# Optimization experiments

Measured on AMD Instinct MI355X. Metric: run time of the kernel, lower is better.

## Reference

```python
import jax, jax.numpy as jnp
import numpy as np

NEG = -1e9  # additive mask value


def _longformer_attn(x, kv_mask, Wq, bq, Wk, bk, Wv, bv, Wqg, bqg, Wkg, bkg, Wvg, bvg, Wo, bo, H, w, G):
    # x: [B, S, E]; kv_mask: [B, S] (mask*-1 > 0 => global; first G tokens are global by construction)
    B, S, E = x.shape
    D = E // H
    scale = 1.0 / float(D) ** 0.5

    def proj(W, b):  # -> [B, H, S, D]
        return (x @ W + b).reshape(B, S, H, D).transpose(0, 2, 1, 3)

    q = proj(Wq, bq) * scale
    k = proj(Wk, bk)
    v = proj(Wv, bv)

    nc = S // w  # number of query chunks of size w
    # banded keys/values: each chunk of w queries sees a 3w key band (prev/cur/next chunk)
    idx = (jnp.arange(nc) * w)[:, None] + jnp.arange(3 * w)[None, :]  # [nc, 3w] into padded seq

    def band(t):  # [B,H,S,D] -> [B,H,nc,3w,D]
        tp = jnp.pad(t, ((0, 0), (0, 0), (w, w), (0, 0)))
        return tp[:, :, idx, :]

    k3, v3 = band(k), band(v)
    qc = q.reshape(B, H, nc, w, D)
    s_win = jnp.einsum('bhcwd,bhced->bhcwe', qc, k3)  # [B,H,nc,w,3w]

    i = jnp.arange(w)[:, None]
    j = jnp.arange(3 * w)[None, :]
    rel_ok = (j >= i) & (j <= i + 2 * w)  # |key_pos - query_pos| <= w
    keypos = (jnp.arange(nc) * w)[:, None, None] + (jnp.arange(3 * w) - w)[None, None, :]  # [nc,1,3w]
    ok = rel_ok[None] & (keypos >= 0) & (keypos < S) & (keypos >= G)  # global keys handled separately
    s_win = jnp.where(ok[None, None], s_win, NEG)

    # every query also attends to the G global keys (standard projections)
    s_g = jnp.einsum('bhqd,bhgd->bhqg', q, k[:, :, :G])  # [B,H,S,G]
    s_all = jnp.concatenate([s_g, s_win.reshape(B, H, S, 3 * w)], axis=-1)
    p = jax.nn.softmax(s_all, axis=-1)  # joint softmax over global + window keys
    p_g, p_w = p[..., :G], p[..., G:].reshape(B, H, nc, w, 3 * w)

    out = jnp.einsum('bhcwe,bhced->bhcwd', p_w, v3).reshape(B, H, S, D)
    out = out + jnp.einsum('bhqg,bhgd->bhqd', p_g, v[:, :, :G])

    # global query rows: full attention over all tokens with the *global* projections
    qg = (x @ Wqg + bqg).reshape(B, S, H, D).transpose(0, 2, 1, 3)[:, :, :G] * scale
    kg = (x @ Wkg + bkg).reshape(B, S, H, D).transpose(0, 2, 1, 3)
    vg = (x @ Wvg + bvg).reshape(B, S, H, D).transpose(0, 2, 1, 3)
    pg = jax.nn.softmax(jnp.einsum('bhgd,bhsd->bhgs', qg, kg), axis=-1)  # [B,H,G,S]
    out = out.at[:, :, :G].set(jnp.einsum('bhgs,bhsd->bhgd', pg, vg))

    ctx = out.transpose(0, 2, 1, 3).reshape(B, S, E)
    return ctx @ Wo + bo  # wrapper's self.output Linear


def setup_inputs() -> dict:
    key = jax.random.key(0)
    B, S, E, H, w, G = 2, 4096, 1024, 16, 256, 64
    ks = jax.random.split(key, 20)
    x = jax.random.normal(ks[0], (B, S, E), dtype=jnp.float32)
    # key_value_states acts as the mask source: (kv * -1) > 0 marks global tokens
    kv = jnp.zeros((B, S), dtype=jnp.float32).at[:, :G].set(-1.0)

    def lin(k1, k2):
        return (jax.random.normal(k1, (E, E), dtype=jnp.float32) * 0.02,
                jax.random.normal(k2, (E,), dtype=jnp.float32) * 0.02)

    Wq, bq = lin(ks[1], ks[2])
    Wk, bk = lin(ks[3], ks[4])
    Wv, bv = lin(ks[5], ks[6])
    Wqg, bqg = lin(ks[7], ks[8])
    Wkg, bkg = lin(ks[9], ks[10])
    Wvg, bvg = lin(ks[11], ks[12])
    Wo, bo = lin(ks[13], ks[14])
    return {"hidden_states": x, "key_value_states": kv,
            "Wq": Wq, "bq": bq, "Wk": Wk, "bk": bk, "Wv": Wv, "bv": bv,
            "Wqg": Wqg, "bqg": bqg, "Wkg": Wkg, "bkg": bkg, "Wvg": Wvg, "bvg": bvg,
            "Wo": Wo, "bo": bo, "num_heads": H, "window": w, "num_global": G}


def reference(hidden_states, key_value_states, Wq, bq, Wk, bk, Wv, bv, Wqg, bqg, Wkg, bkg, Wvg, bvg, Wo, bo, num_heads, window, num_global):
    return _longformer_attn(hidden_states, key_value_states, Wq, bq, Wk, bk, Wv, bv,
                            Wqg, bqg, Wkg, bkg, Wvg, bvg, Wo, bo,
                            num_heads, window, num_global)
```

## Files before the change

### kernel.cpp

```cpp
#include <hip/hip_runtime.h>

typedef _Float16 half_t;
typedef _Float16 h8 __attribute__((ext_vector_type(8)));
typedef _Float16 h4 __attribute__((ext_vector_type(4)));
typedef _Float16 h2 __attribute__((ext_vector_type(2)));
typedef float f4 __attribute__((ext_vector_type(4)));

#define DEV __device__ __forceinline__

constexpr int Bc = 2, Sc = 4096, Ec = 1024, Hc = 16, Dc = 64, Wc = 256, Gc = 64;
constexpr float QSCALE = 0.125f;
constexpr float NEGV = -1e9f;

DEV f4 mfma16(h8 a, h8 b, f4 c) {
  return __builtin_amdgcn_mfma_f32_16x16x32_f16(a, b, c, 0, 0, 0);
}

DEV void gl_lds16(const half_t* g, half_t* l) {
  __builtin_amdgcn_global_load_lds((const __attribute__((address_space(1))) void*)g,
                                   (__attribute__((address_space(3))) void*)l, 16, 0, 0);
}

#define BARx() asm volatile("s_barrier" ::: "memory")
#define VMW(N) asm volatile("s_waitcnt vmcnt(" #N ")" ::: "memory")

__global__ void prep(const float* __restrict__ x,
                     const float* __restrict__ Wq, const float* __restrict__ Wk,
                     const float* __restrict__ Wv, const float* __restrict__ Wkg,
                     const float* __restrict__ Wvg, const float* __restrict__ Wqg,
                     const float* __restrict__ Wo,
                     half_t* __restrict__ xh, half_t* __restrict__ Wcat,
                     half_t* __restrict__ WtO) {
  __shared__ float tile[64][65];
  const int bx = blockIdx.x;
  if (bx < 4096) {
    const int i = bx * 256 + threadIdx.x;
    const float4* x4 = (const float4*)x;
    float4 a = x4[i * 2], b = x4[i * 2 + 1];
    h8 o;
    o[0] = (half_t)a.x; o[1] = (half_t)a.y; o[2] = (half_t)a.z; o[3] = (half_t)a.w;
    o[4] = (half_t)b.x; o[5] = (half_t)b.y; o[6] = (half_t)b.z; o[7] = (half_t)b.w;
    ((h8*)xh)[i] = o;
    return;
  }
  const int widx = bx - 4096;
  const int y = widx >> 8;
  const int xb = widx & 255;
  const float* W = (y == 0) ? Wq : (y == 1) ? Wk : (y == 2) ? Wv :
                   (y == 3) ? Wkg : (y == 4) ? Wvg : (y == 5) ? Wqg : Wo;
  half_t* Wt = (y < 6) ? (Wcat + (size_t)y * Ec * Ec) : WtO;
  const int bxt = xb & 15, byt = xb >> 4;
  const int tx = threadIdx.x & 63, ty = threadIdx.x >> 6;
  const int n0 = bxt * 64, k0 = byt * 64;
#pragma unroll
  for (int i = 0; i < 16; ++i) {
    int k = ty + i * 4;
    tile[k][tx] = W[(size_t)(k0 + k) * Ec + n0 + tx];
  }
  __syncthreads();
  const int tx2 = threadIdx.x & 31, ty2 = threadIdx.x >> 5;
#pragma unroll
  for (int i = 0; i < 8; ++i) {
    const int n = ty2 + i * 8;
    h2 v;
    v[0] = (half_t)tile[2 * tx2][n];
    v[1] = (half_t)tile[2 * tx2 + 1][n];
    *(h2*)(Wt + (size_t)(n0 + n) * Ec + k0 + tx2 * 2) = v;
  }
}

__global__ __launch_bounds__(256, 2) void gemm_proj(const half_t* __restrict__ A,
                                                    const half_t* __restrict__ Bt,
                                                    const float* __restrict__ bq,
                                                    const float* __restrict__ bk,
                                                    const float* __restrict__ bv,
                                                    const float* __restrict__ bkg,
                                                    const float* __restrict__ bvg,
                                                    const float* __restrict__ bqg,
                                                    half_t* __restrict__ qh, half_t* __restrict__ kh,
                                                    half_t* __restrict__ vt, half_t* __restrict__ kgh,
                                                    half_t* __restrict__ vgt, half_t* __restrict__ qgh) {
  __shared__ __align__(16) half_t Ash[3][8192];
  __shared__ __align__(16) half_t Bsh[3][4096];
  const bool qgblk = (blockIdx.y == 32);
  if (qgblk && blockIdx.x >= 8) return;
  const int tid = threadIdx.x;
  const int wv = tid >> 6, lane = tid & 63;
  const int mr = lane & 15, qd = lane >> 4;
  const int wv_m = wv >> 1, wv_n = wv & 1;
  const int col0 = qgblk ? (5 * Ec + (int)blockIdx.x * 128) : (int)blockIdx.x * 128;
  const int row0 = qgblk ? 0 : (int)blockIdx.y * 256;
  const int g = col0 >> 10;

  const half_t* sA[4];
  const half_t* sB[2];
  int dstoA[4], dstoB[2];
#pragma unroll
  for (int j = 0; j < 4; ++j) {
    const int slot = j * 256 + tid;
    const int r = slot >> 2;
    const int kc = (slot & 3) ^ ((r >> 1) & 3);
    int ar;
    if (qgblk) { const int rm = r & 127; ar = (rm < 64) ? rm : 4032 + rm; }
    else ar = row0 + r;
    sA[j] = A + (size_t)ar * Ec + kc * 8;
    dstoA[j] = slot * 8;
  }
#pragma unroll
  for (int j = 0; j < 2; ++j) {
    const int slot = j * 256 + tid;
    const int r = slot >> 2;
    const int kc = (slot & 3) ^ ((r >> 1) & 3);
    sB[j] = Bt + (size_t)(col0 + r) * Ec + kc * 8;
    dstoB[j] = slot * 8;
  }
  int aoff[8], boff[4];
#pragma unroll
  for (int mt = 0; mt < 8; ++mt) {
    const int r = wv_m * 128 + mt * 16 + mr;
    aoff[mt] = ((r << 2) | (qd ^ ((r >> 1) & 3))) * 8;
  }
#pragma unroll
  for (int nt = 0; nt < 4; ++nt) {
    const int r = wv_n * 64 + nt * 16 + mr;
    boff[nt] = ((r << 2) | (qd ^ ((r >> 1) & 3))) * 8;
  }

  f4 acc[8][4] = {};

  auto stage = [&](half_t* da, half_t* db, int k0) {
#pragma unroll
    for (int j = 0; j < 4; ++j) gl_lds16(sA[j] + k0, da + dstoA[j]);
#pragma unroll
    for (int j = 0; j < 2; ++j) gl_lds16(sB[j] + k0, db + dstoB[j]);
  };
  auto compute = [&](const half_t* ba, const half_t* bb) {
    h8 af[8], bf[4];
#pragma unroll
    for (int mt = 0; mt < 8; ++mt) af[mt] = *(const h8*)(ba + aoff[mt]);
#pragma unroll
    for (int nt = 0; nt < 4; ++nt) bf[nt] = *(const h8*)(bb + boff[nt]);
    __builtin_amdgcn_s_setprio(1);
#pragma unroll
    for (int mt = 0; mt < 8; ++mt)
#pragma unroll
      for (int nt = 0; nt < 4; ++nt)
        acc[mt][nt] = mfma16(af[mt], bf[nt], acc[mt][nt]);
    __builtin_amdgcn_s_setprio(0);
  };

  stage(&Ash[0][0], &Bsh[0][0], 0);
  stage(&Ash[1][0], &Bsh[1][0], 32);
  VMW(6);
  BARx();

#pragma unroll 1
  for (int it = 0; it < 10; ++it) {
    const int kk = it * 96;
    stage(&Ash[2][0], &Bsh[2][0], kk + 64);
    compute(&Ash[0][0], &Bsh[0][0]);
    VMW(6); BARx();
    stage(&Ash[0][0], &Bsh[0][0], kk + 96);
    compute(&Ash[1][0], &Bsh[1][0]);
    VMW(6); BARx();
    stage(&Ash[1][0], &Bsh[1][0], kk + 128);
    compute(&Ash[2][0], &Bsh[2][0]);
    VMW(6); BARx();
  }
  compute(&Ash[0][0], &Bsh[0][0]);
  VMW(0);
  BARx();
  compute(&Ash[1][0], &Bsh[1][0]);

  const float* bptr = (g == 0) ? bq : (g == 1) ? bk : (g == 2) ? bv :
                      (g == 3) ? bkg : (g == 4) ? bvg : bqg;
#pragma unroll
  for (int mt = 0; mt < 8; ++mt) {
#pragma unroll
    for (int nt = 0; nt < 4; ++nt) {
      const int C = col0 + wv_n * 64 + nt * 16 + mr;
      const int c1 = C & 1023, hh = c1 >> 6, d = c1 & 63;
      const float bval = bptr[c1];
      const int Rbase = row0 + wv_m * 128 + mt * 16 + qd * 4;
      f4 a = acc[mt][nt];
      if (g == 2 || g == 4) {
        half_t* O = (g == 2) ? vt : vgt;
        int b = Rbase >> 12, s = Rbase & 4095;
        h4 pk;
#pragma unroll
        for (int r = 0; r < 4; ++r) pk[r] = (half_t)(a[r] + bval);
        *(h4*)(O + ((size_t)(b * Hc + hh) * Dc + d) * Sc + s) = pk;
      } else if (g == 5) {
#pragma unroll
        for (int r = 0; r < 4; ++r) {
          int rr = Rbase + r;
          if (rr < 128) {
            int b = rr >> 6, s = rr & 63;
            qgh[((size_t)(b * Hc + hh) * Gc + s) * Dc + d] = (half_t)((a[r] + bval) * QSCALE);
          }
        }
      } else {
        half_t* O = (g == 0) ? qh : (g == 1) ? kh : kgh;
        const float scale = (g == 0) ? QSCALE : 1.0f;
#pragma unroll
        for (int r = 0; r < 4; ++r) {
          int R = Rbase + r;
          int b = R >> 12, s = R & 4095;
          O[((size_t)(b * Hc + hh) * Sc + s) * Dc + d] = (half_t)((a[r] + bval) * scale);
        }
      }
    }
  }
}

__global__ __launch_bounds__(256, 3) void gemm_out(const half_t* __restrict__ A,
                                                   const half_t* __restrict__ Bt,
                                                   const float* __restrict__ bias,
                                                   float* __restrict__ O) {
  __shared__ __align__(16) half_t Ash[3][4096];
  __shared__ __align__(16) half_t Bsh[3][4096];
  const int tid = threadIdx.x;
  const int wv = tid >> 6, lane = tid & 63;
  const int mr = lane & 15, qd = lane >> 4;
  const int wv_m = wv >> 1, wv_n = wv & 1;
  const int col0 = blockIdx.x * 128;
  const int row0 = blockIdx.y * 128;

  const half_t* sA[2];
  const half_t* sB[2];
  int dsto[2];
#pragma unroll
  for (int i = 0; i < 2; ++i) {
    const int slot = wv * 128 + i * 64 + lane;
    const int r = slot >> 2;
    const int kc = (slot & 3) ^ ((r >> 1) & 3);
    sA[i] = A + (size_t)(row0 + r) * Ec + kc * 8;
    sB[i] = Bt + (size_t)(col0 + r) * Ec + kc * 8;
    dsto[i] = (wv * 128 + i * 64) * 8;
  }
  int aoff[4], boff[4];
#pragma unroll
  for (int mt = 0; mt < 4; ++mt) {
    const int r = wv_m * 64 + mt * 16 + mr;
    aoff[mt] = ((r << 2) | (qd ^ ((r >> 1) & 3))) * 8;
  }
#pragma unroll
  for (int nt = 0; nt < 4; ++nt) {
    const int r = wv_n * 64 + nt * 16 + mr;
    boff[nt] = ((r << 2) | (qd ^ ((r >> 1) & 3))) * 8;
  }

  f4 acc[4][4] = {};

  auto stage = [&](half_t* da, half_t* db, int k0) {
#pragma unroll
    for (int i = 0; i < 2; ++i) {
      gl_lds16(sA[i] + k0, da + dsto[i]);
      gl_lds16(sB[i] + k0, db + dsto[i]);
    }
  };
  auto compute = [&](const half_t* ba, const half_t* bb) {
    h8 af[4], bf[4];
#pragma unroll
    for (int mt = 0; mt < 4; ++mt) af[mt] = *(const h8*)(ba + aoff[mt]);
#pragma unroll
    for (int nt = 0; nt < 4; ++nt) bf[nt] = *(const h8*)(bb + boff[nt]);
    __builtin_amdgcn_s_setprio(1);
#pragma unroll
    for (int mt = 0; mt < 4; ++mt)
#pragma unroll
      for (int nt = 0; nt < 4; ++nt)
        acc[mt][nt] = mfma16(af[mt], bf[nt], acc[mt][nt]);
    __builtin_amdgcn_s_setprio(0);
  };

  stage(&Ash[0][0], &Bsh[0][0], 0);
  stage(&Ash[1][0], &Bsh[1][0], 32);
  VMW(4);
  BARx();

#pragma unroll 1
  for (int it = 0; it < 10; ++it) {
    const int kk = it * 96;
    stage(&Ash[2][0], &Bsh[2][0], kk + 64);
    compute(&Ash[0][0], &Bsh[0][0]);
    VMW(4); BARx();
    stage(&Ash[0][0], &Bsh[0][0], kk + 96);
    compute(&Ash[1][0], &Bsh[1][0]);
    VMW(4); BARx();
    stage(&Ash[1][0], &Bsh[1][0], kk + 128);
    compute(&Ash[2][0], &Bsh[2][0]);
    VMW(4); BARx();
  }
  compute(&Ash[0][0], &Bsh[0][0]);
  VMW(0);
  BARx();
  compute(&Ash[1][0], &Bsh[1][0]);

#pragma unroll
  for (int mt = 0; mt < 4; ++mt) {
#pragma unroll
    for (int nt = 0; nt < 4; ++nt) {
      const int C = col0 + wv_n * 64 + nt * 16 + mr;
      const float bval = bias[C];
      const int Rbase = row0 + wv_m * 64 + mt * 16 + qd * 4;
      f4 a = acc[mt][nt];
#pragma unroll
      for (int r = 0; r < 4; ++r)
        O[(size_t)(Rbase + r) * Ec + C] = a[r] + bval;
    }
  }
}

__global__ __launch_bounds__(256) void attn_fused(const half_t* __restrict__ qh,
                                                  const half_t* __restrict__ kh,
                                                  const half_t* __restrict__ vt,
                                                  const half_t* __restrict__ qgh,
                                                  const half_t* __restrict__ kgh,
                                                  const half_t* __restrict__ vgt,
                                                  half_t* __restrict__ ctx,
                                                  float* __restrict__ pm,
                                                  float* __restrict__ pl,
                                                  float* __restrict__ pacc) {
  constexpr int PST = 88;
  __shared__ __align__(16) half_t Kb[2][64 * 64];
  __shared__ __align__(16) half_t Vb[2][64 * 64];
  __shared__ __align__(16) half_t Pl[4][16 * PST];
  const int bid0 = blockIdx.x;
  const int tid = threadIdx.x, wv = tid >> 6, lane = tid & 63;
  const int mr = lane & 15, qd = lane >> 4;
  half_t* Pw = &Pl[wv][0];

  if (bid0 >= 512) {
    const int gb = bid0 - 512;
    const int ch = gb & 7, h = (gb >> 3) & 15, b = gb >> 7;
    const size_t bh = (size_t)(b * Hc + h);
    const half_t* qb = qgh + bh * Gc * Dc;
    const half_t* kb = kgh + bh * Sc * Dc;
    const half_t* vb = vgt + bh * Dc * Sc;

    const int qrow = wv * 16 + mr;
    const h8 qf0 = *(const h8*)(qb + (size_t)qrow * Dc + qd * 8);
    const h8 qf1 = *(const h8*)(qb + (size_t)qrow * Dc + 32 + qd * 8);

    float m_run = -1e30f, l_run = 0.f;
    f4 acc[4] = {};

    for (int t = 0; t < 8; ++t) {
      const int kp0 = ch * 512 + t * 64;
      f4 sa[4];
#pragma unroll
      for (int mt = 0; mt < 4; ++mt) {
        const int kp = kp0 + mt * 16 + mr;
        h8 kf0 = *(const h8*)(kb + (size_t)kp * Dc + qd * 8);
        h8 kf1 = *(const h8*)(kb + (size_t)kp * Dc + 32 + qd * 8);
        f4 s = {};
        s = mfma16(kf0, qf0, s);
        s = mfma16(kf1, qf1, s);
        sa[mt] = s;
      }
      float tm = -1e30f;
#pragma unroll
      for (int mt = 0; mt < 4; ++mt)
#pragma unroll
        for (int r = 0; r < 4; ++r) tm = fmaxf(tm, sa[mt][r]);
      tm = fmaxf(tm, __shfl_xor(tm, 16));
      tm = fmaxf(tm, __shfl_xor(tm, 32));
      const float mnew = fmaxf(m_run, tm);
      const float alpha = __expf(m_run - mnew);
      m_run = mnew;
      float psum = 0.0f;
#pragma unroll
      for (int mt = 0; mt < 4; ++mt) {
        h4 pk;
#pragma unroll
        for (int r = 0; r < 4; ++r) {
          const float p = __expf(sa[mt][r] - mnew);
          psum += p;
          pk[r] = (half_t)p;
        }
        *(h4*)(Pw + mr * PST + mt * 16 + qd * 4) = pk;
      }
      psum += __shfl_xor(psum, 16);
      psum += __shfl_xor(psum, 32);
      l_run = l_run * alpha + psum;
#pragma unroll
      for (int mt = 0; mt < 4; ++mt)
#pragma unroll
        for (int r = 0; r < 4; ++r) acc[mt][r] *= alpha;
      const h8 p0 = *(const h8*)(Pw + mr * PST + qd * 8);
      const h8 p1 = *(const h8*)(Pw + mr * PST + 32 + qd * 8);
#pragma unroll
      for (int mt = 0; mt < 4; ++mt) {
        const h8 vf0 = *(const h8*)(vb + (size_t)(mt * 16 + mr) * Sc + kp0 + qd * 8);
        const h8 vf1 = *(const h8*)(vb + (size_t)(mt * 16 + mr) * Sc + kp0 + 32 + qd * 8);
        acc[mt] = mfma16(vf0, p0, acc[mt]);
        acc[mt] = mfma16(vf1, p1, acc[mt]);
      }
    }

    const size_t pidx = (bh * 8 + ch) * Gc + qrow;
    if (qd == 0) { pm[pidx] = m_run; pl[pidx] = l_run; }
    float* pa = pacc + pidx * Dc;
#pragma unroll
    for (int mt = 0; mt < 4; ++mt)
#pragma unroll
      for (int r = 0; r < 4; ++r)
        pa[mt * 16 + qd * 4 + r] = acc[mt][r];
    return;
  }

  const int qc = bid0 & 15, h = (bid0 >> 4) & 15, b = bid0 >> 8;
  const int qs = qc << 8;
  const int qw = qs + wv * 64;
  const size_t bh = (size_t)(b * Hc + h);
  const half_t* qb = qh + bh * Sc * Dc;
  const half_t* kb = kh + bh * Sc * Dc;
  const half_t* vb = vt + bh * Dc * Sc;

  h8 qf[4][2];
#pragma unroll
  for (int qt = 0; qt < 4; ++qt) {
    const half_t* qrow = qb + (size_t)(qw + qt * 16 + mr) * Dc;
    qf[qt][0] = *(const h8*)(qrow + qd * 8);
    qf[qt][1] = *(const h8*)(qrow + 32 + qd * 8);
  }

  int tiles[14];
  int nT = 0;
  tiles[nT++] = 0;
  {
    int lo = qs - Wc; if (lo < Gc) lo = Gc;
    int hi2 = qs + 448; if (hi2 > Sc - 64) hi2 = Sc - 64;
    for (int kp0 = lo; kp0 <= hi2; kp0 += 64) tiles[nT++] = kp0;
  }

  auto stage = [&](int kp0, int bi) {
#pragma unroll
    for (int i = 0; i < 2; ++i) {
      const int seg = wv * 2 + i;
      const int s = seg * 64 + lane;
      const int r = s >> 3;
      const int kc = (s & 7) ^ (r & 7);
      gl_lds16(kb + (size_t)(kp0 + r) * Dc + kc * 8, &Kb[bi][seg * 512]);
      gl_lds16(vb + (size_t)r * Sc + kp0 + kc * 8, &Vb[bi][seg * 512]);
    }
  };

  float m_run[4], l_run[4];
  f4 acc[4][4] = {};
#pragma unroll
  for (int qt = 0; qt < 4; ++qt) { m_run[qt] = -1e30f; l_run[qt] = 0.f; }

  stage(tiles[0], 0);

  for (int t = 0; t < nT; ++t) {
    __syncthreads();
    if (t + 1 < nT) stage(tiles[t + 1], (t + 1) & 1);
    const int kp0 = tiles[t];
    if (t > 0 && (kp0 > qw + 319 || kp0 + 63 < qw - Wc)) continue;

    const half_t* BK = Kb[t & 1];
    const half_t* BV = Vb[t & 1];
    h8 kf[4][2], vf[4][2];
#pragma unroll
    for (int mt = 0; mt < 4; ++mt) {
      const int row = mt * 16 + mr, r7 = row & 7;
      kf[mt][0] = *(const h8*)(BK + (size_t)(row * 8 + (qd ^ r7)) * 8);
      kf[mt][1] = *(const h8*)(BK + (size_t)(row * 8 + ((qd + 4) ^ r7)) * 8);
      vf[mt][0] = *(const h8*)(BV + (size_t)(row * 8 + (qd ^ r7)) * 8);
      vf[mt][1] = *(const h8*)(BV + (size_t)(row * 8 + ((qd + 4) ^ r7)) * 8);
    }
    const bool nomask = (t == 0) || (kp0 >= qw - 193 && kp0 <= qw + 193);

#pragma unroll
    for (int qt = 0; qt < 4; ++qt) {
      f4 sa[4];
#pragma unroll
      for (int mt = 0; mt < 4; ++mt) {
        f4 s = {};
        s = mfma16(kf[mt][0], qf[qt][0], s);
        s = mfma16(kf[mt][1], qf[qt][1], s);
        sa[mt] = s;
      }
      const int q = qw + qt * 16 + mr;
      if (!nomask) {
#pragma unroll
        for (int mt = 0; mt < 4; ++mt)
#pragma unroll
          for (int r = 0; r < 4; ++r) {
            const int kp = kp0 + mt * 16 + qd * 4 + r;
            if (kp < q - Wc || kp > q + Wc) sa[mt][r] = NEGV;
          }
      }
      float tm = -1e30f;
#pragma unroll
      for (int mt = 0; mt < 4; ++mt)
#pragma unroll
        for (int r = 0; r < 4; ++r) tm = fmaxf(tm, sa[mt][r]);
      tm = fmaxf(tm, __shfl_xor(tm, 16));
      tm = fmaxf(tm, __shfl_xor(tm, 32));
      const float mnew = fmaxf(m_run[qt], tm);
      const float alpha = __expf(m_run[qt] - mnew);
      m_run[qt] = mnew;
      float psum = 0.0f;
#pragma unroll
      for (int mt = 0; mt < 4; ++mt) {
        h4 pk;
#pragma unroll
        for (int r = 0; r < 4; ++r) {
          const float p = __expf(sa[mt][r] - mnew);
          psum += p;
          pk[r] = (half_t)p;
        }
        *(h4*)(Pw + mr * PST + mt * 16 + qd * 4) = pk;
      }
      psum += __shfl_xor(psum, 16);
      psum += __shfl_xor(psum, 32);
      l_run[qt] = l_run[qt] * alpha + psum;
#pragma unroll
      for (int mt = 0; mt < 4; ++mt)
#pragma unroll
        for (int r = 0; r < 4; ++r) acc[qt][mt][r] *= alpha;
      const h8 p0 = *(const h8*)(Pw + mr * PST + qd * 8);
      const h8 p1 = *(const h8*)(Pw + mr * PST + 32 + qd * 8);
#pragma unroll
      for (int mt = 0; mt < 4; ++mt) {
        acc[qt][mt] = mfma16(vf[mt][0], p0, acc[qt][mt]);
        acc[qt][mt] = mfma16(vf[mt][1], p1, acc[qt][mt]);
      }
    }
  }

#pragma unroll
  for (int qt = 0; qt < 4; ++qt) {
    const float inv = 1.0f / l_run[qt];
    const int q = qw + qt * 16 + mr;
    half_t* crow = ctx + ((size_t)(b * Sc) + q) * Ec + h * Dc;
#pragma unroll
    for (int mt = 0; mt < 4; ++mt) {
      h4 pk;
#pragma unroll
      for (int r = 0; r < 4; ++r) pk[r] = (half_t)(acc[qt][mt][r] * inv);
      *(h4*)(crow + mt * 16 + qd * 4) = pk;
    }
  }
}

__global__ __launch_bounds__(256) void gq_combine(const float* __restrict__ pm,
                                                  const float* __restrict__ pl,
                                                  const float* __restrict__ pacc,
                                                  half_t* __restrict__ ctx) {
  const int h = blockIdx.x & 15, b = blockIdx.x >> 4;
  const size_t bh = (size_t)(b * Hc + h);
  const int q = threadIdx.x >> 2, dg = (threadIdx.x & 3) * 16;
  float m[8];
  float M = -1e30f;
#pragma unroll
  for (int c = 0; c < 8; ++c) {
    m[c] = pm[(bh * 8 + c) * Gc + q];
    M = fmaxf(M, m[c]);
  }
  float denom = 0.f, num[16] = {};
#pragma unroll
  for (int c = 0; c < 8; ++c) {
    const float w = __expf(m[c] - M);
    denom += w * pl[(bh * 8 + c) * Gc + q];
    const float* pa = pacc + ((bh * 8 + c) * Gc + q) * Dc + dg;
#pragma unroll
    for (int j = 0; j < 16; ++j) num[j] += w * pa[j];
  }
  const float inv = 1.0f / denom;
  half_t* crow = ctx + ((size_t)(b * Sc) + q) * Ec + h * Dc + dg;
#pragma unroll
  for (int j = 0; j < 16; ++j) crow[j] = (half_t)(num[j] * inv);
}


extern "C" void kernel_launch(void* const* d_in, const int* in_sizes, int n_in,
                              void* d_out, int out_size, void* d_ws, size_t ws_size,
                              hipStream_t stream) {
  const float* x   = (const float*)d_in[0];
  const float* Wq  = (const float*)d_in[2];
  const float* bq  = (const float*)d_in[3];
  const float* Wk  = (const float*)d_in[4];
  const float* bk  = (const float*)d_in[5];
  const float* Wv  = (const float*)d_in[6];
  const float* bv  = (const float*)d_in[7];
  const float* Wqg = (const float*)d_in[8];
  const float* bqg = (const float*)d_in[9];
  const float* Wkg = (const float*)d_in[10];
  const float* bkg = (const float*)d_in[11];
  const float* Wvg = (const float*)d_in[12];
  const float* bvg = (const float*)d_in[13];
  const float* Wo  = (const float*)d_in[14];
  const float* bo  = (const float*)d_in[15];
  float* out = (float*)d_out;

  char* ws = (char*)d_ws;
  size_t off = 0;
  auto alloc = [&](size_t bytes) {
    void* p = ws + off;
    off = (off + bytes + 255) & ~(size_t)255;
    return p;
  };
  const size_t BSE2 = (size_t)Bc * Sc * Ec * 2;
  const size_t W2 = (size_t)Ec * Ec * 2;
  half_t* xh   = (half_t*)alloc(BSE2);
  half_t* Wcat = (half_t*)alloc(W2 * 6);
  half_t* WtO  = (half_t*)alloc(W2);
  half_t* qh   = (half_t*)alloc(BSE2);
  half_t* kh   = (half_t*)alloc(BSE2);
  half_t* vt   = (half_t*)alloc(BSE2);
  half_t* kgh  = (half_t*)alloc(BSE2);
  half_t* vgt  = (half_t*)alloc(BSE2);
  half_t* qgh  = (half_t*)alloc((size_t)Bc * Hc * Gc * Dc * 2);
  half_t* ctx  = (half_t*)alloc(BSE2);
  float*  pm   = (float*)alloc((size_t)Bc * Hc * 8 * Gc * 4);
  float*  pl   = (float*)alloc((size_t)Bc * Hc * 8 * Gc * 4);
  float*  pacc = (float*)alloc((size_t)Bc * Hc * 8 * Gc * Dc * 4);
  (void)ws_size; (void)in_sizes; (void)n_in; (void)out_size;

  prep<<<4096 + 7 * 256, 256, 0, stream>>>(x, Wq, Wk, Wv, Wkg, Wvg, Wqg, Wo,
                                           xh, Wcat, WtO);

  gemm_proj<<<dim3(40, 33), 256, 0, stream>>>(xh, Wcat, bq, bk, bv, bkg, bvg, bqg,
                                              qh, kh, vt, kgh, vgt, qgh);

  attn_fused<<<512 + 256, 256, 0, stream>>>(qh, kh, vt, qgh, kgh, vgt,
                                            ctx, pm, pl, pacc);

  gq_combine<<<Bc * Hc, 256, 0, stream>>>(pm, pl, pacc, ctx);

  gemm_out<<<dim3(8, 64), 256, 0, stream>>>(ctx, WtO, bo, out);
}
```

Baseline: 394.2 us.

## Drop split-K for global-query attention and fuse combine into attention kernel

Global-query attention blocks now each process a full (batch, head) over all keys instead of eight key chunks, and write normalized context directly. This removes the gq_combine kernel launch and the fp32 partial buffers. Local blocks skip writing rows belonging to global queries to avoid overwriting. The trade-off is fewer, longer global blocks that may lengthen the tail of the attention kernel.

```diff
diff --git a/kernel.cpp b/kernel.cpp
--- a/kernel.cpp
+++ b/kernel.cpp
@@ -318,10 +318,7 @@
                                                   const half_t* __restrict__ qgh,
                                                   const half_t* __restrict__ kgh,
                                                   const half_t* __restrict__ vgt,
-                                                  half_t* __restrict__ ctx,
-                                                  float* __restrict__ pm,
-                                                  float* __restrict__ pl,
-                                                  float* __restrict__ pacc) {
+                                                  half_t* __restrict__ ctx) {
   constexpr int PST = 88;
   __shared__ __align__(16) half_t Kb[2][64 * 64];
   __shared__ __align__(16) half_t Vb[2][64 * 64];
@@ -333,7 +330,7 @@
 
   if (bid0 >= 512) {
     const int gb = bid0 - 512;
-    const int ch = gb & 7, h = (gb >> 3) & 15, b = gb >> 7;
+    const int h = gb & 15, b = gb >> 4;
     const size_t bh = (size_t)(b * Hc + h);
     const half_t* qb = qgh + bh * Gc * Dc;
     const half_t* kb = kgh + bh * Sc * Dc;
@@ -346,8 +343,9 @@
     float m_run = -1e30f, l_run = 0.f;
     f4 acc[4] = {};
 
-    for (int t = 0; t < 8; ++t) {
-      const int kp0 = ch * 512 + t * 64;
+#pragma unroll 1
+    for (int t = 0; t < 64; ++t) {
+      const int kp0 = t * 64;
       f4 sa[4];
 #pragma unroll
       for (int mt = 0; mt < 4; ++mt) {
@@ -399,14 +397,15 @@
       }
     }
 
-    const size_t pidx = (bh * 8 + ch) * Gc + qrow;
-    if (qd == 0) { pm[pidx] = m_run; pl[pidx] = l_run; }
-    float* pa = pacc + pidx * Dc;
-#pragma unroll
-    for (int mt = 0; mt < 4; ++mt)
-#pragma unroll
-      for (int r = 0; r < 4; ++r)
-        pa[mt * 16 + qd * 4 + r] = acc[mt][r];
+    const float inv = 1.0f / l_run;
+    half_t* crow = ctx + ((size_t)(b * Sc) + qrow) * Ec + h * Dc;
+#pragma unroll
+    for (int mt = 0; mt < 4; ++mt) {
+      h4 pk;
+#pragma unroll
+      for (int r = 0; r < 4; ++r) pk[r] = (half_t)(acc[mt][r] * inv);
+      *(h4*)(crow + mt * 16 + qd * 4) = pk;
+    }
     return;
   }
 
@@ -536,44 +535,17 @@
   for (int qt = 0; qt < 4; ++qt) {
     const float inv = 1.0f / l_run[qt];
     const int q = qw + qt * 16 + mr;
-    half_t* crow = ctx + ((size_t)(b * Sc) + q) * Ec + h * Dc;
-#pragma unroll
-    for (int mt = 0; mt < 4; ++mt) {
-      h4 pk;
-#pragma unroll
-      for (int r = 0; r < 4; ++r) pk[r] = (half_t)(acc[qt][mt][r] * inv);
-      *(h4*)(crow + mt * 16 + qd * 4) = pk;
-    }
-  }
-}
-
-__global__ __launch_bounds__(256) void gq_combine(const float* __restrict__ pm,
-                                                  const float* __restrict__ pl,
-                                                  const float* __restrict__ pacc,
-                                                  half_t* __restrict__ ctx) {
-  const int h = blockIdx.x & 15, b = blockIdx.x >> 4;
-  const size_t bh = (size_t)(b * Hc + h);
-  const int q = threadIdx.x >> 2, dg = (threadIdx.x & 3) * 16;
-  float m[8];
-  float M = -1e30f;
-#pragma unroll
-  for (int c = 0; c < 8; ++c) {
-    m[c] = pm[(bh * 8 + c) * Gc + q];
-    M = fmaxf(M, m[c]);
-  }
-  float denom = 0.f, num[16] = {};
-#pragma unroll
-  for (int c = 0; c < 8; ++c) {
-    const float w = __expf(m[c] - M);
-    denom += w * pl[(bh * 8 + c) * Gc + q];
-    const float* pa = pacc + ((bh * 8 + c) * Gc + q) * Dc + dg;
-#pragma unroll
-    for (int j = 0; j < 16; ++j) num[j] += w * pa[j];
-  }
-  const float inv = 1.0f / denom;
-  half_t* crow = ctx + ((size_t)(b * Sc) + q) * Ec + h * Dc + dg;
-#pragma unroll
-  for (int j = 0; j < 16; ++j) crow[j] = (half_t)(num[j] * inv);
+    if (q >= Gc) {
+      half_t* crow = ctx + ((size_t)(b * Sc) + q) * Ec + h * Dc;
+#pragma unroll
+      for (int mt = 0; mt < 4; ++mt) {
+        h4 pk;
+#pragma unroll
+        for (int r = 0; r < 4; ++r) pk[r] = (half_t)(acc[qt][mt][r] * inv);
+        *(h4*)(crow + mt * 16 + qd * 4) = pk;
+      }
+    }
+  }
 }
 
 
@@ -616,9 +588,6 @@
   half_t* vgt  = (half_t*)alloc(BSE2);
   half_t* qgh  = (half_t*)alloc((size_t)Bc * Hc * Gc * Dc * 2);
   half_t* ctx  = (half_t*)alloc(BSE2);
-  float*  pm   = (float*)alloc((size_t)Bc * Hc * 8 * Gc * 4);
-  float*  pl   = (float*)alloc((size_t)Bc * Hc * 8 * Gc * 4);
-  float*  pacc = (float*)alloc((size_t)Bc * Hc * 8 * Gc * Dc * 4);
   (void)ws_size; (void)in_sizes; (void)n_in; (void)out_size;
 
   prep<<<4096 + 7 * 256, 256, 0, stream>>>(x, Wq, Wk, Wv, Wkg, Wvg, Wqg, Wo,
@@ -627,10 +596,7 @@
   gemm_proj<<<dim3(40, 33), 256, 0, stream>>>(xh, Wcat, bq, bk, bv, bkg, bvg, bqg,
                                               qh, kh, vt, kgh, vgt, qgh);
 
-  attn_fused<<<512 + 256, 256, 0, stream>>>(qh, kh, vt, qgh, kgh, vgt,
-                                            ctx, pm, pl, pacc);
-
-  gq_combine<<<Bc * Hc, 256, 0, stream>>>(pm, pl, pacc, ctx);
+  attn_fused<<<512 + 32, 256, 0, stream>>>(qh, kh, vt, qgh, kgh, vgt, ctx);
 
   gemm_out<<<dim3(8, 64), 256, 0, stream>>>(ctx, WtO, bo, out);
 }
```

Measured after the change: 479.1 us. 21.5% more time.
